# Kernel tuning notes

Measured on AMD Instinct MI355X. Metric: run time of the kernel, lower is better.

The kernel has to match this reference:

```python
import jax, jax.numpy as jnp
import numpy as np

B, N, C = 4, 4000, 91          # images, proposals/image, classes (incl. background)
H = W = 800                    # image shape
WX, WY, WW, WH = 10.0, 10.0, 5.0, 5.0   # bbox_reg_weights
BBOX_CLIP = float(np.log(1000.0 / 16.0))
SCORE_T = 0.05
NMS_T = 0.5
DETS = 100                     # detections_per_img
MIN_SIZE = 0.01
NEG = jnp.float32(-1e30)
M = N * (C - 1)                # candidates per image after dropping background


def setup_inputs() -> dict:
    key = jax.random.key(0)
    k1, k2, k3, k4 = jax.random.split(key, 4)
    class_logits = jax.random.normal(k1, (B * N, C), jnp.float32)
    box_regression = jax.random.normal(k2, (B * N, C * 4), jnp.float32)
    # valid proposals: x1<x2, y1<y2, inside the image
    ctr = jax.random.uniform(k3, (B, N, 2), jnp.float32, 0.0, 800.0)
    wh = jax.random.uniform(k4, (B, N, 2), jnp.float32, 16.0, 256.0)
    x1y1 = jnp.clip(ctr - 0.5 * wh, 0.0, 800.0)
    x2y2 = jnp.clip(ctr + 0.5 * wh, 0.0, 800.0)
    proposals = jnp.concatenate([x1y1, x2y2], axis=-1)
    return {"class_logits": class_logits, "box_regression": box_regression,
            "proposals": proposals}


def _decode(rel, props):
    # rel: [B,N,C,4] deltas, props: [B,N,4] -> per-class boxes [B,N,C,4]
    widths = props[..., 2] - props[..., 0]
    heights = props[..., 3] - props[..., 1]
    ctr_x = props[..., 0] + 0.5 * widths
    ctr_y = props[..., 1] + 0.5 * heights
    dx = rel[..., 0] / WX
    dy = rel[..., 1] / WY
    dw = jnp.minimum(rel[..., 2] / WW, BBOX_CLIP)
    dh = jnp.minimum(rel[..., 3] / WH, BBOX_CLIP)
    pcx = dx * widths[..., None] + ctr_x[..., None]
    pcy = dy * heights[..., None] + ctr_y[..., None]
    pw = jnp.exp(dw) * widths[..., None]
    ph = jnp.exp(dh) * heights[..., None]
    return jnp.stack([pcx - 0.5 * pw, pcy - 0.5 * ph,
                      pcx + 0.5 * pw, pcy + 0.5 * ph], axis=-1)


def _iou_one(box, boxes):
    # box [4] vs boxes [M,4]
    lt = jnp.maximum(box[:2], boxes[:, :2])
    rb = jnp.minimum(box[2:], boxes[:, 2:])
    wh = jnp.clip(rb - lt, 0.0)
    inter = wh[:, 0] * wh[:, 1]
    a1 = (box[2] - box[0]) * (box[3] - box[1])
    a2 = (boxes[:, 2] - boxes[:, 0]) * (boxes[:, 3] - boxes[:, 1])
    return inter / (a1 + a2 - inter)


def _nms_image(boxes_off, scores_m):
    # greedy NMS on class-offset boxes; returns DETS indices + validity flags
    idxs = jnp.arange(scores_m.shape[0])

    def step(scores_rem, _):
        best = jnp.argmax(scores_rem)
        bscore = scores_rem[best]
        iou = _iou_one(boxes_off[best], boxes_off)
        sup = (iou > NMS_T) | (idxs == best)
        return jnp.where(sup, NEG, scores_rem), (best, bscore > NEG * 0.5)

    _, (keep_idx, keep_ok) = jax.lax.scan(step, scores_m, None, length=DETS)
    return keep_idx, keep_ok


def reference(class_logits, box_regression, proposals):
    logits = class_logits.reshape(B, N, C)
    rel = box_regression.reshape(B, N, C, 4)
    boxes = _decode(rel, proposals)                       # [B,N,C,4]
    # clip_boxes_to_image
    boxes = jnp.stack([jnp.clip(boxes[..., 0], 0.0, W),
                       jnp.clip(boxes[..., 1], 0.0, H),
                       jnp.clip(boxes[..., 2], 0.0, W),
                       jnp.clip(boxes[..., 3], 0.0, H)], axis=-1)
    scores = jax.nn.softmax(logits, axis=-1)              # [B,N,C]
    # drop background class 0, flatten per-image candidates
    cand_boxes = boxes[:, :, 1:, :].reshape(B, M, 4)
    cand_scores = scores[:, :, 1:].reshape(B, M)
    labels = jnp.tile(jnp.arange(1, C, dtype=jnp.int32), N)   # [M]
    # score threshold + remove_small_boxes
    ws = cand_boxes[..., 2] - cand_boxes[..., 0]
    hs = cand_boxes[..., 3] - cand_boxes[..., 1]
    valid = (cand_scores > SCORE_T) & (ws >= MIN_SIZE) & (hs >= MIN_SIZE)
    scores_m = jnp.where(valid, cand_scores, NEG)
    # batched_nms: offset boxes per class so cross-class boxes never overlap
    offs = labels.astype(jnp.float32) * (W + 1.0)
    boxes_off = cand_boxes + offs[None, :, None]
    keep_idx, keep_ok = jax.vmap(_nms_image)(boxes_off, scores_m)  # [B,DETS]
    out_boxes = jnp.take_along_axis(cand_boxes, keep_idx[..., None], axis=1)
    out_scores = jnp.take_along_axis(cand_scores, keep_idx, axis=1)
    out_labels = labels[keep_idx]
    out_boxes = jnp.where(keep_ok[..., None], out_boxes, 0.0)
    out_scores = jnp.where(keep_ok, out_scores, 0.0)
    out_labels = jnp.where(keep_ok, out_labels, 0)
    return out_boxes, out_scores, out_labels, keep_ok
```

## Files before the change

kernel.cpp:

```cpp
#include <hip/hip_runtime.h>

#define Bc 4
#define Nc 4000
#define Cc 91
#define SEGW 20
#define BCAP 64
#define SELTGT 512
#define DETS 100
#define NBIN 4096
#define SELCAP 1024

typedef unsigned long long u64;

__device__ __forceinline__ float4 decode_box(const float4 r, float w, float h,
                                             float cx, float cy) {
    const float BBOX_CLIP = 4.135166556742356f;
    float dx = r.x / 10.f, dy = r.y / 10.f;
    float dw = fminf(r.z / 5.f, BBOX_CLIP);
    float dh = fminf(r.w / 5.f, BBOX_CLIP);
    float pcx = dx * w + cx, pcy = dy * h + cy;
    float pw = expf(dw) * w, ph = expf(dh) * h;
    float4 o;
    o.x = fminf(fmaxf(pcx - 0.5f * pw, 0.f), 800.f);
    o.y = fminf(fmaxf(pcy - 0.5f * ph, 0.f), 800.f);
    o.z = fminf(fmaxf(pcx + 0.5f * pw, 0.f), 800.f);
    o.w = fminf(fmaxf(pcy + 0.5f * ph, 0.f), 800.f);
    return o;
}

__global__ __launch_bounds__(256) void compact_k(
    const float* __restrict__ logits, const float* __restrict__ regs,
    const float* __restrict__ props, ulonglong2* __restrict__ pmask,
    unsigned* __restrict__ scoreseg, int* __restrict__ ghist) {
    if (blockIdx.x < 16) {
        int base = blockIdx.x * 1024;
#pragma unroll
        for (int j = 0; j < 4; ++j)
            ghist[base + j * 256 + threadIdx.x] = 0;
    }
    const int wv = threadIdx.x >> 6;
    const int ln = threadIdx.x & 63;
    const int pA = blockIdx.x * 8 + wv * 2;
    const int pB = pA + 1;

    const float* lA = logits + (size_t)pA * Cc;
    const float* lB = logits + (size_t)pB * Cc;
    float a0 = lA[ln];
    float b0 = lB[ln];
    float a1 = (ln < Cc - 64) ? lA[64 + ln] : -1e30f;
    float b1 = (ln < Cc - 64) ? lB[64 + ln] : -1e30f;
    const float4 prA = *reinterpret_cast<const float4*>(props + 4 * (size_t)pA);
    const float4 prB = *reinterpret_cast<const float4*>(props + 4 * (size_t)pB);

    float mA = fmaxf(a0, a1), mB = fmaxf(b0, b1);
#pragma unroll
    for (int off = 32; off; off >>= 1) {
        mA = fmaxf(mA, __shfl_xor(mA, off));
        mB = fmaxf(mB, __shfl_xor(mB, off));
    }
    float eA0 = expf(a0 - mA), eB0 = expf(b0 - mB);
    float eA1 = (ln < Cc - 64) ? expf(a1 - mA) : 0.f;
    float eB1 = (ln < Cc - 64) ? expf(b1 - mB) : 0.f;
    float sA = eA0 + eA1, sB = eB0 + eB1;
#pragma unroll
    for (int off = 32; off; off >>= 1) {
        sA += __shfl_xor(sA, off);
        sB += __shfl_xor(sB, off);
    }

    const float wA = prA.z - prA.x, hA = prA.w - prA.y;
    const float cxA = prA.x + 0.5f * wA, cyA = prA.y + 0.5f * hA;
    const float wB = prB.z - prB.x, hB = prB.w - prB.y;
    const float cxB = prB.x + 0.5f * wB, cyB = prB.y + 0.5f * hB;

    float vA0 = eA0 / sA, vB0 = eB0 / sB, vA1 = eA1 / sA, vB1 = eB1 / sB;
    bool fA0 = false, fA1 = false, fB0 = false, fB1 = false;
    if (ln >= 1 && vA0 > 0.05f) {
        float4 r = *reinterpret_cast<const float4*>(
            regs + ((size_t)pA * Cc + ln) * 4);
        float4 bx = decode_box(r, wA, hA, cxA, cyA);
        fA0 = (bx.z - bx.x >= 0.01f) && (bx.w - bx.y >= 0.01f);
    }
    if (ln >= 1 && vB0 > 0.05f) {
        float4 r = *reinterpret_cast<const float4*>(
            regs + ((size_t)pB * Cc + ln) * 4);
        float4 bx = decode_box(r, wB, hB, cxB, cyB);
        fB0 = (bx.z - bx.x >= 0.01f) && (bx.w - bx.y >= 0.01f);
    }
    if (ln < Cc - 64 && vA1 > 0.05f) {
        float4 r = *reinterpret_cast<const float4*>(
            regs + ((size_t)pA * Cc + 64 + ln) * 4);
        float4 bx = decode_box(r, wA, hA, cxA, cyA);
        fA1 = (bx.z - bx.x >= 0.01f) && (bx.w - bx.y >= 0.01f);
    }
    if (ln < Cc - 64 && vB1 > 0.05f) {
        float4 r = *reinterpret_cast<const float4*>(
            regs + ((size_t)pB * Cc + 64 + ln) * 4);
        float4 bx = decode_box(r, wB, hB, cxB, cyB);
        fB1 = (bx.z - bx.x >= 0.01f) && (bx.w - bx.y >= 0.01f);
    }

    const u64 below = (1ULL << ln) - 1ULL;
    u64 mA0 = __ballot(fA0), mA1 = __ballot(fA1);
    u64 mB0 = __ballot(fB0), mB1 = __ballot(fB1);
    int cA0 = __popcll(mA0), cB0 = __popcll(mB0);
    if (fA0) scoreseg[(size_t)pA * SEGW + __popcll(mA0 & below)] =
        __float_as_uint(vA0);
    if (fA1) scoreseg[(size_t)pA * SEGW + cA0 + __popcll(mA1 & below)] =
        __float_as_uint(vA1);
    if (fB0) scoreseg[(size_t)pB * SEGW + __popcll(mB0 & below)] =
        __float_as_uint(vB0);
    if (fB1) scoreseg[(size_t)pB * SEGW + cB0 + __popcll(mB1 & below)] =
        __float_as_uint(vB1);
    if (ln == 0) {
        pmask[pA] = make_ulonglong2(mA0, mA1);
        pmask[pB] = make_ulonglong2(mB0, mB1);
    }
}

__global__ __launch_bounds__(256) void hist_k(
    const ulonglong2* __restrict__ pmask, const unsigned* __restrict__ scoreseg,
    int* __restrict__ ghist) {
    __shared__ int hist[NBIN];
    const int b = blockIdx.x >> 4;
    const int sub = blockIdx.x & 15;
    const int t = threadIdx.x;
    for (int i = t; i < NBIN; i += 256) hist[i] = 0;
    __syncthreads();
    if (t < 250) {
        int p = b * Nc + sub * 250 + t;
        ulonglong2 pm = pmask[p];
        int nk = __popcll(pm.x) + __popcll(pm.y);
        for (int j = 0; j < nk; ++j)
            atomicAdd(&hist[scoreseg[(size_t)p * SEGW + j] >> 20], 1);
    }
    __syncthreads();
    for (int i = t; i < NBIN; i += 256) {
        int v = hist[i];
        if (v) atomicAdd(&ghist[b * NBIN + i], v);
    }
}

__global__ __launch_bounds__(256) void thresh_k(const int* __restrict__ ghist,
                                               int* __restrict__ thr,
                                               int* __restrict__ bcnt) {
    {
        const int t = threadIdx.x;
        if (t < Bc * Cc - 256) bcnt[256 + t] = 0;
        bcnt[t] = 0;
    }
    const int wv = threadIdx.x >> 6;
    const int ln = threadIdx.x & 63;
    const int* h = ghist + wv * NBIN;
    int loc[64];
    int tot = 0;
#pragma unroll
    for (int j = 0; j < 64; ++j) { loc[j] = h[ln * 64 + j]; tot += loc[j]; }
    int inc = tot;
#pragma unroll
    for (int off = 1; off < 64; off <<= 1) {
        int v = __shfl_down(inc, off);
        if (ln + off < 64) inc += v;
    }
    int cum = inc - tot;
    int myThr = -1;
#pragma unroll
    for (int j = 63; j >= 0; --j) {
        if (cum < SELTGT && cum + loc[j] >= SELTGT) myThr = ln * 64 + j;
        cum += loc[j];
    }
#pragma unroll
    for (int off = 32; off; off >>= 1)
        myThr = max(myThr, __shfl_xor(myThr, off));
    if (ln == 0) thr[wv] = (myThr < 0) ? 0 : myThr;
}

__global__ __launch_bounds__(256) void select_k(
    const ulonglong2* __restrict__ pmask, const unsigned* __restrict__ scoreseg,
    const int* __restrict__ thr, u64* __restrict__ bucket,
    int* __restrict__ bcnt) {
    const int p = blockIdx.x * 256 + threadIdx.x;
    if (p >= Bc * Nc) return;
    const ulonglong2 pm = pmask[p];
    if ((pm.x | pm.y) == 0ULL) return;
    const int b = p / Nc;
    const int n = p - b * Nc;
    const int th = thr[b];
    int idx = 0;
#pragma unroll
    for (int rnd = 0; rnd < 2; ++rnd) {
        u64 mm = rnd ? pm.y : pm.x;
        while (mm) {
            int j = __ffsll((long long)mm) - 1; mm &= mm - 1;
            int c = j + rnd * 64;
            unsigned sb = scoreseg[(size_t)p * SEGW + idx]; ++idx;
            if ((int)(sb >> 20) >= th) {
                unsigned m = (unsigned)(n * 90 + (c - 1));
                u64 key = ((u64)sb << 32) | ((u64)(1048575u - m) << 12) | (u64)c;
                int sl = atomicAdd(&bcnt[b * Cc + c], 1);
                if (sl < BCAP) bucket[(b * Cc + c) * BCAP + sl] = key;
            }
        }
    }
}

__global__ __launch_bounds__(64) void nmsc_k(
    u64* __restrict__ bucket, const int* __restrict__ bcnt,
    const float* __restrict__ regs, const float* __restrict__ props,
    int* __restrict__ kkc) {
    const int b = blockIdx.x / (Cc - 1);
    const int c = 1 + blockIdx.x % (Cc - 1);
    const int ln = threadIdx.x;
    const int nc = min(bcnt[b * Cc + c], BCAP);
    bool alive = ln < nc;
    u64 lk = alive ? bucket[(b * Cc + c) * BCAP + ln] : 0ULL;
    float4 bx = make_float4(0.f, 0.f, 0.f, 0.f);
    float area = 0.f;
    if (alive) {
        int m = 1048575 - (int)((lk >> 12) & 0xFFFFFULL);
        int n = m / (Cc - 1);
        int p = b * Nc + n;
        const float4 pr = *reinterpret_cast<const float4*>(props + 4 * (size_t)p);
        float w = pr.z - pr.x, h = pr.w - pr.y;
        float cx = pr.x + 0.5f * w, cy = pr.y + 0.5f * h;
        const float4 r = *reinterpret_cast<const float4*>(
            regs + ((size_t)p * Cc + c) * 4);
        bx = decode_box(r, w, h, cx, cy);
        float off_ = (float)c * 801.0f;
        bx.x += off_; bx.y += off_; bx.z += off_; bx.w += off_;
        area = (bx.z - bx.x) * (bx.w - bx.y);
    }

    int nk = 0;
    for (;;) {
        u64 m = alive ? lk : 0ULL;
#pragma unroll
        for (int off = 32; off; off >>= 1) {
            u64 o = __shfl_xor(m, off);
            m = (o > m) ? o : m;
        }
        if (m == 0ULL) break;
        u64 wmask = __ballot(alive && lk == m);
        int wl = __ffsll((long long)wmask) - 1;
        if (ln == wl) bucket[(b * Cc + c) * BCAP + nk] = m;
        ++nk;
        float wx1 = __shfl(bx.x, wl), wy1 = __shfl(bx.y, wl);
        float wx2 = __shfl(bx.z, wl), wy2 = __shfl(bx.w, wl);
        float wa = __shfl(area, wl);
        if (alive) {
            if (lk == m) {
                alive = false;
            } else {
                float iw = fmaxf(fminf(wx2, bx.z) - fmaxf(wx1, bx.x), 0.f);
                float ih = fmaxf(fminf(wy2, bx.w) - fmaxf(wy1, bx.y), 0.f);
                float inter = iw * ih;
                float iou = inter / (wa + area - inter);
                if (iou > 0.5f) alive = false;
            }
        }
    }
    if (ln == 0) kkc[b * Cc + c] = nk;
}

__global__ __launch_bounds__(1024) void top100_k(
    const u64* __restrict__ bucket, const int* __restrict__ kkc,
    const float* __restrict__ regs, const float* __restrict__ props,
    float* __restrict__ out) {
    __shared__ u64 sKey[SELCAP];
    __shared__ u64 sTop[DETS];
    __shared__ int cnts[Cc], offs[Cc + 1];
    const int b = blockIdx.x, t = threadIdx.x;
    const int ln = t & 63, wv = t >> 6;

    if (t < Cc)
        cnts[t] = (t == 0) ? 0 : min(max(kkc[b * Cc + t], 0), BCAP);
    if (t < DETS) sTop[t] = 0ULL;
    __syncthreads();
    if (t == 0) {
        int acc = 0;
        for (int c = 0; c < Cc; ++c) { offs[c] = acc; acc += cnts[c]; }
        offs[Cc] = acc;
    }
    __syncthreads();
    const int total = min(offs[Cc], SELCAP);

    for (int c = wv; c < Cc; c += 16) {
        int k = cnts[c];
        if (ln < k) {
            int d = offs[c] + ln;
            if (d >= 0 && d < SELCAP)
                sKey[d] = bucket[(b * Cc + c) * BCAP + ln];
        }
    }
    __syncthreads();

    for (int i = t; i < total; i += 1024) {
        u64 k = sKey[i];
        int r = 0;
#pragma unroll 4
        for (int j = 0; j < total; ++j) r += (sKey[j] > k) ? 1 : 0;
        if (r < DETS) sTop[r] = k;
    }
    __syncthreads();

    if (t < DETS) {
        int o = b * DETS + t;
        u64 k = sTop[t];
        float* ob = out + (size_t)o * 4;
        if (k != 0ULL) {
            int lab = (int)(k & 0xFFFULL);
            int m = 1048575 - (int)((k >> 12) & 0xFFFFFULL);
            int n = m / (Cc - 1);
            int c = m - n * (Cc - 1) + 1;
            int p = b * Nc + n;
            const float4 pr =
                *reinterpret_cast<const float4*>(props + 4 * (size_t)p);
            const float w = pr.z - pr.x, h = pr.w - pr.y;
            const float cx = pr.x + 0.5f * w, cy = pr.y + 0.5f * h;
            const float4 r4 = *reinterpret_cast<const float4*>(
                regs + ((size_t)p * Cc + c) * 4);
            float4 bx = decode_box(r4, w, h, cx, cy);
            ob[0] = bx.x; ob[1] = bx.y; ob[2] = bx.z; ob[3] = bx.w;
            out[Bc * DETS * 4 + o] = __uint_as_float((unsigned)(k >> 32));
            out[Bc * DETS * 5 + o] = (float)lab;
            out[Bc * DETS * 6 + o] = 1.0f;
        } else {
            ob[0] = ob[1] = ob[2] = ob[3] = 0.f;
            out[Bc * DETS * 4 + o] = 0.f;
            out[Bc * DETS * 5 + o] = 0.f;
            out[Bc * DETS * 6 + o] = 0.f;
        }
    }
}

extern "C" void kernel_launch(void* const* d_in, const int* in_sizes, int n_in,
                              void* d_out, int out_size, void* d_ws, size_t ws_size,
                              hipStream_t stream) {
    const float* logits = (const float*)d_in[0];
    const float* regs   = (const float*)d_in[1];
    const float* props  = (const float*)d_in[2];
    float* out = (float*)d_out;

    char* ws = (char*)d_ws;
    size_t o = 0;
    ulonglong2* pmask = (ulonglong2*)(ws + o); o += (size_t)Bc * Nc * 16;
    unsigned* scoreseg = (unsigned*)(ws + o);  o += (size_t)Bc * Nc * SEGW * 4;
    u64* bucket  = (u64*)(ws + o);             o += (size_t)Bc * Cc * BCAP * 8;
    int* ghist   = (int*)(ws + o);             o += (size_t)Bc * NBIN * 4;
    int* bcnt    = (int*)(ws + o);             o += (size_t)Bc * Cc * 4;
    int* kkc     = (int*)(ws + o);             o += (size_t)Bc * Cc * 4;
    int* thr     = (int*)(ws + o);

    hipLaunchKernelGGL(compact_k, dim3(Bc * Nc / 8), dim3(256), 0, stream,
                       logits, regs, props, pmask, scoreseg, ghist);
    hipLaunchKernelGGL(hist_k, dim3(Bc * 16), dim3(256), 0, stream,
                       pmask, scoreseg, ghist);
    hipLaunchKernelGGL(thresh_k, dim3(1), dim3(256), 0, stream, ghist, thr, bcnt);
    hipLaunchKernelGGL(select_k, dim3((Bc * Nc + 255) / 256), dim3(256), 0,
                       stream, pmask, scoreseg, thr, bucket, bcnt);
    hipLaunchKernelGGL(nmsc_k, dim3(Bc * (Cc - 1)), dim3(64), 0, stream,
                       bucket, bcnt, regs, props, kkc);
    hipLaunchKernelGGL(top100_k, dim3(Bc), dim3(1024), 0, stream,
                       bucket, kkc, regs, props, out);
}
```

Baseline: 55.73 us.

## Fuse threshold into select and per-class NMS into top-100 kernel

Cuts the pipeline from six launches to four. Each select block now recomputes its image's histogram threshold itself, and the per-class NMS runs inside the per-image top-100 kernel, using shared-memory buckets loaded once. bcnt zeroing moves into compact_k. This removes launch and inter-kernel gaps, but NMS now runs on only 4 blocks of 16 waves, each wave looping over about 6 classes serially, instead of 360 parallel single-wave blocks. The per-block threshold scan is also repeated 16 times per image.

```diff
diff --git a/kernel.cpp b/kernel.cpp
--- a/kernel.cpp
+++ b/kernel.cpp
@@ -31,12 +31,17 @@
 __global__ __launch_bounds__(256) void compact_k(
     const float* __restrict__ logits, const float* __restrict__ regs,
     const float* __restrict__ props, ulonglong2* __restrict__ pmask,
-    unsigned* __restrict__ scoreseg, int* __restrict__ ghist) {
+    unsigned* __restrict__ scoreseg, int* __restrict__ ghist,
+    int* __restrict__ bcnt) {
     if (blockIdx.x < 16) {
         int base = blockIdx.x * 1024;
 #pragma unroll
         for (int j = 0; j < 4; ++j)
             ghist[base + j * 256 + threadIdx.x] = 0;
+    } else if (blockIdx.x == 16) {
+        int t = threadIdx.x;
+        bcnt[t] = 0;
+        if (t < Bc * Cc - 256) bcnt[256 + t] = 0;
     }
     const int wv = threadIdx.x >> 6;
     const int ln = threadIdx.x & 63;
@@ -141,155 +146,155 @@
     }
 }
 
-__global__ __launch_bounds__(256) void thresh_k(const int* __restrict__ ghist,
-                                               int* __restrict__ thr,
-                                               int* __restrict__ bcnt) {
-    {
-        const int t = threadIdx.x;
-        if (t < Bc * Cc - 256) bcnt[256 + t] = 0;
-        bcnt[t] = 0;
-    }
-    const int wv = threadIdx.x >> 6;
-    const int ln = threadIdx.x & 63;
-    const int* h = ghist + wv * NBIN;
-    int loc[64];
-    int tot = 0;
-#pragma unroll
-    for (int j = 0; j < 64; ++j) { loc[j] = h[ln * 64 + j]; tot += loc[j]; }
-    int inc = tot;
-#pragma unroll
-    for (int off = 1; off < 64; off <<= 1) {
-        int v = __shfl_down(inc, off);
-        if (ln + off < 64) inc += v;
-    }
-    int cum = inc - tot;
-    int myThr = -1;
-#pragma unroll
-    for (int j = 63; j >= 0; --j) {
-        if (cum < SELTGT && cum + loc[j] >= SELTGT) myThr = ln * 64 + j;
-        cum += loc[j];
-    }
-#pragma unroll
-    for (int off = 32; off; off >>= 1)
-        myThr = max(myThr, __shfl_xor(myThr, off));
-    if (ln == 0) thr[wv] = (myThr < 0) ? 0 : myThr;
-}
-
-__global__ __launch_bounds__(256) void select_k(
+__global__ __launch_bounds__(256) void selthr_k(
     const ulonglong2* __restrict__ pmask, const unsigned* __restrict__ scoreseg,
-    const int* __restrict__ thr, u64* __restrict__ bucket,
+    const int* __restrict__ ghist, u64* __restrict__ bucket,
     int* __restrict__ bcnt) {
-    const int p = blockIdx.x * 256 + threadIdx.x;
-    if (p >= Bc * Nc) return;
-    const ulonglong2 pm = pmask[p];
-    if ((pm.x | pm.y) == 0ULL) return;
-    const int b = p / Nc;
-    const int n = p - b * Nc;
-    const int th = thr[b];
-    int idx = 0;
-#pragma unroll
-    for (int rnd = 0; rnd < 2; ++rnd) {
-        u64 mm = rnd ? pm.y : pm.x;
-        while (mm) {
-            int j = __ffsll((long long)mm) - 1; mm &= mm - 1;
-            int c = j + rnd * 64;
-            unsigned sb = scoreseg[(size_t)p * SEGW + idx]; ++idx;
-            if ((int)(sb >> 20) >= th) {
-                unsigned m = (unsigned)(n * 90 + (c - 1));
-                u64 key = ((u64)sb << 32) | ((u64)(1048575u - m) << 12) | (u64)c;
-                int sl = atomicAdd(&bcnt[b * Cc + c], 1);
-                if (sl < BCAP) bucket[(b * Cc + c) * BCAP + sl] = key;
+    __shared__ int thrS;
+    const int b = blockIdx.x >> 4;
+    const int sub = blockIdx.x & 15;
+    const int t = threadIdx.x;
+
+    if (t < 64) {
+        const int ln = t;
+        const int* h = ghist + b * NBIN;
+        int loc[64];
+        int tot = 0;
+#pragma unroll
+        for (int j = 0; j < 64; ++j) { loc[j] = h[ln * 64 + j]; tot += loc[j]; }
+        int inc = tot;
+#pragma unroll
+        for (int off = 1; off < 64; off <<= 1) {
+            int v = __shfl_down(inc, off);
+            if (ln + off < 64) inc += v;
+        }
+        int cum = inc - tot;
+        int myThr = -1;
+#pragma unroll
+        for (int j = 63; j >= 0; --j) {
+            if (cum < SELTGT && cum + loc[j] >= SELTGT) myThr = ln * 64 + j;
+            cum += loc[j];
+        }
+#pragma unroll
+        for (int off = 32; off; off >>= 1)
+            myThr = max(myThr, __shfl_xor(myThr, off));
+        if (ln == 0) thrS = (myThr < 0) ? 0 : myThr;
+    }
+    __syncthreads();
+    const int th = thrS;
+
+    if (t < 250) {
+        int p = b * Nc + sub * 250 + t;
+        const ulonglong2 pm = pmask[p];
+        if (pm.x | pm.y) {
+            const int n = p - b * Nc;
+            int idx = 0;
+#pragma unroll
+            for (int rnd = 0; rnd < 2; ++rnd) {
+                u64 mm = rnd ? pm.y : pm.x;
+                while (mm) {
+                    int j = __ffsll((long long)mm) - 1; mm &= mm - 1;
+                    int c = j + rnd * 64;
+                    unsigned sb = scoreseg[(size_t)p * SEGW + idx]; ++idx;
+                    if ((int)(sb >> 20) >= th) {
+                        unsigned m = (unsigned)(n * 90 + (c - 1));
+                        u64 key = ((u64)sb << 32) |
+                                  ((u64)(1048575u - m) << 12) | (u64)c;
+                        int sl = atomicAdd(&bcnt[b * Cc + c], 1);
+                        if (sl < BCAP) bucket[(b * Cc + c) * BCAP + sl] = key;
+                    }
+                }
             }
         }
     }
 }
 
-__global__ __launch_bounds__(64) void nmsc_k(
-    u64* __restrict__ bucket, const int* __restrict__ bcnt,
-    const float* __restrict__ regs, const float* __restrict__ props,
-    int* __restrict__ kkc) {
-    const int b = blockIdx.x / (Cc - 1);
-    const int c = 1 + blockIdx.x % (Cc - 1);
-    const int ln = threadIdx.x;
-    const int nc = min(bcnt[b * Cc + c], BCAP);
-    bool alive = ln < nc;
-    u64 lk = alive ? bucket[(b * Cc + c) * BCAP + ln] : 0ULL;
-    float4 bx = make_float4(0.f, 0.f, 0.f, 0.f);
-    float area = 0.f;
-    if (alive) {
-        int m = 1048575 - (int)((lk >> 12) & 0xFFFFFULL);
-        int n = m / (Cc - 1);
-        int p = b * Nc + n;
-        const float4 pr = *reinterpret_cast<const float4*>(props + 4 * (size_t)p);
-        float w = pr.z - pr.x, h = pr.w - pr.y;
-        float cx = pr.x + 0.5f * w, cy = pr.y + 0.5f * h;
-        const float4 r = *reinterpret_cast<const float4*>(
-            regs + ((size_t)p * Cc + c) * 4);
-        bx = decode_box(r, w, h, cx, cy);
-        float off_ = (float)c * 801.0f;
-        bx.x += off_; bx.y += off_; bx.z += off_; bx.w += off_;
-        area = (bx.z - bx.x) * (bx.w - bx.y);
-    }
-
-    int nk = 0;
-    for (;;) {
-        u64 m = alive ? lk : 0ULL;
-#pragma unroll
-        for (int off = 32; off; off >>= 1) {
-            u64 o = __shfl_xor(m, off);
-            m = (o > m) ? o : m;
-        }
-        if (m == 0ULL) break;
-        u64 wmask = __ballot(alive && lk == m);
-        int wl = __ffsll((long long)wmask) - 1;
-        if (ln == wl) bucket[(b * Cc + c) * BCAP + nk] = m;
-        ++nk;
-        float wx1 = __shfl(bx.x, wl), wy1 = __shfl(bx.y, wl);
-        float wx2 = __shfl(bx.z, wl), wy2 = __shfl(bx.w, wl);
-        float wa = __shfl(area, wl);
-        if (alive) {
-            if (lk == m) {
-                alive = false;
-            } else {
-                float iw = fmaxf(fminf(wx2, bx.z) - fmaxf(wx1, bx.x), 0.f);
-                float ih = fmaxf(fminf(wy2, bx.w) - fmaxf(wy1, bx.y), 0.f);
-                float inter = iw * ih;
-                float iou = inter / (wa + area - inter);
-                if (iou > 0.5f) alive = false;
-            }
-        }
-    }
-    if (ln == 0) kkc[b * Cc + c] = nk;
-}
-
-__global__ __launch_bounds__(1024) void top100_k(
-    const u64* __restrict__ bucket, const int* __restrict__ kkc,
+__global__ __launch_bounds__(1024) void nmstop_k(
+    const u64* __restrict__ bucket, const int* __restrict__ bcnt,
     const float* __restrict__ regs, const float* __restrict__ props,
     float* __restrict__ out) {
+    __shared__ u64 sBkt[Cc][BCAP];
     __shared__ u64 sKey[SELCAP];
     __shared__ u64 sTop[DETS];
-    __shared__ int cnts[Cc], offs[Cc + 1];
+    __shared__ int cnts[Cc], kk[Cc], offs[Cc + 1];
     const int b = blockIdx.x, t = threadIdx.x;
     const int ln = t & 63, wv = t >> 6;
 
-    if (t < Cc)
-        cnts[t] = (t == 0) ? 0 : min(max(kkc[b * Cc + t], 0), BCAP);
+    if (t < Cc) cnts[t] = min(max(bcnt[b * Cc + t], 0), BCAP);
     if (t < DETS) sTop[t] = 0ULL;
-    __syncthreads();
+    for (int i = t; i < Cc * BCAP; i += 1024)
+        sBkt[0][i] = bucket[(size_t)b * Cc * BCAP + i];
+    __syncthreads();
+
+    for (int cm1 = wv; cm1 < Cc - 1; cm1 += 16) {
+        const int c = cm1 + 1;
+        const int nc = cnts[c];
+        bool alive = ln < nc;
+        u64 lk = alive ? sBkt[c][ln] : 0ULL;
+        float4 bx = make_float4(0.f, 0.f, 0.f, 0.f);
+        float area = 0.f;
+        if (alive) {
+            int m = 1048575 - (int)((lk >> 12) & 0xFFFFFULL);
+            int n = m / (Cc - 1);
+            int p = b * Nc + n;
+            const float4 pr =
+                *reinterpret_cast<const float4*>(props + 4 * (size_t)p);
+            float w = pr.z - pr.x, h = pr.w - pr.y;
+            float cx = pr.x + 0.5f * w, cy = pr.y + 0.5f * h;
+            const float4 r = *reinterpret_cast<const float4*>(
+                regs + ((size_t)p * Cc + c) * 4);
+            bx = decode_box(r, w, h, cx, cy);
+            float off_ = (float)c * 801.0f;
+            bx.x += off_; bx.y += off_; bx.z += off_; bx.w += off_;
+            area = (bx.z - bx.x) * (bx.w - bx.y);
+        }
+        int nk = 0;
+        for (;;) {
+            u64 m = alive ? lk : 0ULL;
+#pragma unroll
+            for (int off = 32; off; off >>= 1) {
+                u64 o = __shfl_xor(m, off);
+                m = (o > m) ? o : m;
+            }
+            if (m == 0ULL) break;
+            u64 wmask = __ballot(alive && lk == m);
+            int wl = __ffsll((long long)wmask) - 1;
+            if (ln == wl) sBkt[c][nk] = m;
+            ++nk;
+            float wx1 = __shfl(bx.x, wl), wy1 = __shfl(bx.y, wl);
+            float wx2 = __shfl(bx.z, wl), wy2 = __shfl(bx.w, wl);
+            float wa = __shfl(area, wl);
+            if (alive) {
+                if (lk == m) {
+                    alive = false;
+                } else {
+                    float iw = fmaxf(fminf(wx2, bx.z) - fmaxf(wx1, bx.x), 0.f);
+                    float ih = fmaxf(fminf(wy2, bx.w) - fmaxf(wy1, bx.y), 0.f);
+                    float inter = iw * ih;
+                    float iou = inter / (wa + area - inter);
+                    if (iou > 0.5f) alive = false;
+                }
+            }
+        }
+        if (ln == 0) kk[c] = nk;
+    }
+    __syncthreads();
+
     if (t == 0) {
         int acc = 0;
-        for (int c = 0; c < Cc; ++c) { offs[c] = acc; acc += cnts[c]; }
+        offs[0] = 0;
+        for (int c = 1; c < Cc; ++c) { offs[c] = acc; acc += kk[c]; }
         offs[Cc] = acc;
     }
     __syncthreads();
     const int total = min(offs[Cc], SELCAP);
 
-    for (int c = wv; c < Cc; c += 16) {
-        int k = cnts[c];
+    for (int cm1 = wv; cm1 < Cc - 1; cm1 += 16) {
+        const int c = cm1 + 1;
+        int k = kk[c];
         if (ln < k) {
             int d = offs[c] + ln;
-            if (d >= 0 && d < SELCAP)
-                sKey[d] = bucket[(b * Cc + c) * BCAP + ln];
+            if (d >= 0 && d < SELCAP) sKey[d] = sBkt[c][ln];
         }
     }
     __syncthreads();
@@ -348,18 +353,13 @@
     u64* bucket  = (u64*)(ws + o);             o += (size_t)Bc * Cc * BCAP * 8;
     int* ghist   = (int*)(ws + o);             o += (size_t)Bc * NBIN * 4;
     int* bcnt    = (int*)(ws + o);             o += (size_t)Bc * Cc * 4;
-    int* kkc     = (int*)(ws + o);             o += (size_t)Bc * Cc * 4;
-    int* thr     = (int*)(ws + o);
 
     hipLaunchKernelGGL(compact_k, dim3(Bc * Nc / 8), dim3(256), 0, stream,
-                       logits, regs, props, pmask, scoreseg, ghist);
+                       logits, regs, props, pmask, scoreseg, ghist, bcnt);
     hipLaunchKernelGGL(hist_k, dim3(Bc * 16), dim3(256), 0, stream,
                        pmask, scoreseg, ghist);
-    hipLaunchKernelGGL(thresh_k, dim3(1), dim3(256), 0, stream, ghist, thr, bcnt);
-    hipLaunchKernelGGL(select_k, dim3((Bc * Nc + 255) / 256), dim3(256), 0,
-                       stream, pmask, scoreseg, thr, bucket, bcnt);
-    hipLaunchKernelGGL(nmsc_k, dim3(Bc * (Cc - 1)), dim3(64), 0, stream,
-                       bucket, bcnt, regs, props, kkc);
-    hipLaunchKernelGGL(top100_k, dim3(Bc), dim3(1024), 0, stream,
-                       bucket, kkc, regs, props, out);
-}
+    hipLaunchKernelGGL(selthr_k, dim3(Bc * 16), dim3(256), 0, stream,
+                       pmask, scoreseg, ghist, bucket, bcnt);
+    hipLaunchKernelGGL(nmstop_k, dim3(Bc), dim3(1024), 0, stream,
+                       bucket, bcnt, regs, props, out);
+}
```

Measured after the change: 81.26 us. 1.46x slower.

## Fuse histogram, threshold and select kernels using a grid-wide atomic barrier

Applied to the files above, without the earlier changes.

Merges hist_k, thresh_k and select_k into one kernel of 64 blocks. The blocks synchronise through a global done counter with a spin-wait, then each block computes its image's threshold locally and selects candidates from its own proposal slice. Zeroing of bcnt and the done counter moves into compact_k. This removes two kernel launches and their gaps, but relies on all 64 blocks being co-resident and adds spin-wait and redundant threshold work in each block.

```diff
diff --git a/kernel.cpp b/kernel.cpp
--- a/kernel.cpp
+++ b/kernel.cpp
@@ -31,12 +31,18 @@
 __global__ __launch_bounds__(256) void compact_k(
     const float* __restrict__ logits, const float* __restrict__ regs,
     const float* __restrict__ props, ulonglong2* __restrict__ pmask,
-    unsigned* __restrict__ scoreseg, int* __restrict__ ghist) {
+    unsigned* __restrict__ scoreseg, int* __restrict__ ghist,
+    int* __restrict__ bcnt, int* __restrict__ done) {
     if (blockIdx.x < 16) {
         int base = blockIdx.x * 1024;
 #pragma unroll
         for (int j = 0; j < 4; ++j)
             ghist[base + j * 256 + threadIdx.x] = 0;
+    } else if (blockIdx.x == 16) {
+        int t = threadIdx.x;
+        bcnt[t] = 0;
+        if (t < Bc * Cc - 256) bcnt[256 + t] = 0;
+        if (t == 0) *done = 0;
     }
     const int wv = threadIdx.x >> 6;
     const int ln = threadIdx.x & 63;
@@ -118,13 +124,16 @@
     }
 }
 
-__global__ __launch_bounds__(256) void hist_k(
+__global__ __launch_bounds__(256) void histsel_k(
     const ulonglong2* __restrict__ pmask, const unsigned* __restrict__ scoreseg,
-    int* __restrict__ ghist) {
+    int* __restrict__ ghist, int* __restrict__ done,
+    u64* __restrict__ bucket, int* __restrict__ bcnt) {
     __shared__ int hist[NBIN];
+    __shared__ int thrS;
     const int b = blockIdx.x >> 4;
     const int sub = blockIdx.x & 15;
     const int t = threadIdx.x;
+
     for (int i = t; i < NBIN; i += 256) hist[i] = 0;
     __syncthreads();
     if (t < 250) {
@@ -139,66 +148,65 @@
         int v = hist[i];
         if (v) atomicAdd(&ghist[b * NBIN + i], v);
     }
-}
-
-__global__ __launch_bounds__(256) void thresh_k(const int* __restrict__ ghist,
-                                               int* __restrict__ thr,
-                                               int* __restrict__ bcnt) {
-    {
-        const int t = threadIdx.x;
-        if (t < Bc * Cc - 256) bcnt[256 + t] = 0;
-        bcnt[t] = 0;
-    }
-    const int wv = threadIdx.x >> 6;
-    const int ln = threadIdx.x & 63;
-    const int* h = ghist + wv * NBIN;
-    int loc[64];
-    int tot = 0;
-#pragma unroll
-    for (int j = 0; j < 64; ++j) { loc[j] = h[ln * 64 + j]; tot += loc[j]; }
-    int inc = tot;
-#pragma unroll
-    for (int off = 1; off < 64; off <<= 1) {
-        int v = __shfl_down(inc, off);
-        if (ln + off < 64) inc += v;
-    }
-    int cum = inc - tot;
-    int myThr = -1;
-#pragma unroll
-    for (int j = 63; j >= 0; --j) {
-        if (cum < SELTGT && cum + loc[j] >= SELTGT) myThr = ln * 64 + j;
-        cum += loc[j];
-    }
-#pragma unroll
-    for (int off = 32; off; off >>= 1)
-        myThr = max(myThr, __shfl_xor(myThr, off));
-    if (ln == 0) thr[wv] = (myThr < 0) ? 0 : myThr;
-}
-
-__global__ __launch_bounds__(256) void select_k(
-    const ulonglong2* __restrict__ pmask, const unsigned* __restrict__ scoreseg,
-    const int* __restrict__ thr, u64* __restrict__ bucket,
-    int* __restrict__ bcnt) {
-    const int p = blockIdx.x * 256 + threadIdx.x;
-    if (p >= Bc * Nc) return;
-    const ulonglong2 pm = pmask[p];
-    if ((pm.x | pm.y) == 0ULL) return;
-    const int b = p / Nc;
-    const int n = p - b * Nc;
-    const int th = thr[b];
-    int idx = 0;
-#pragma unroll
-    for (int rnd = 0; rnd < 2; ++rnd) {
-        u64 mm = rnd ? pm.y : pm.x;
-        while (mm) {
-            int j = __ffsll((long long)mm) - 1; mm &= mm - 1;
-            int c = j + rnd * 64;
-            unsigned sb = scoreseg[(size_t)p * SEGW + idx]; ++idx;
-            if ((int)(sb >> 20) >= th) {
-                unsigned m = (unsigned)(n * 90 + (c - 1));
-                u64 key = ((u64)sb << 32) | ((u64)(1048575u - m) << 12) | (u64)c;
-                int sl = atomicAdd(&bcnt[b * Cc + c], 1);
-                if (sl < BCAP) bucket[(b * Cc + c) * BCAP + sl] = key;
+    __syncthreads();
+
+    if (t == 0) {
+        __threadfence();
+        atomicAdd(done, 1);
+        while (atomicAdd(done, 0) < 64) __builtin_amdgcn_s_sleep(8);
+        __threadfence();
+    }
+    __syncthreads();
+
+    if (t < 64) {
+        const int ln = t;
+        const int* h = ghist + b * NBIN;
+        int loc[64];
+        int tot = 0;
+#pragma unroll
+        for (int j = 0; j < 64; ++j) { loc[j] = h[ln * 64 + j]; tot += loc[j]; }
+        int inc = tot;
+#pragma unroll
+        for (int off = 1; off < 64; off <<= 1) {
+            int v = __shfl_down(inc, off);
+            if (ln + off < 64) inc += v;
+        }
+        int cum = inc - tot;
+        int myThr = -1;
+#pragma unroll
+        for (int j = 63; j >= 0; --j) {
+            if (cum < SELTGT && cum + loc[j] >= SELTGT) myThr = ln * 64 + j;
+            cum += loc[j];
+        }
+#pragma unroll
+        for (int off = 32; off; off >>= 1)
+            myThr = max(myThr, __shfl_xor(myThr, off));
+        if (ln == 0) thrS = (myThr < 0) ? 0 : myThr;
+    }
+    __syncthreads();
+    const int th = thrS;
+
+    if (t < 250) {
+        int p = b * Nc + sub * 250 + t;
+        const ulonglong2 pm = pmask[p];
+        if (pm.x | pm.y) {
+            const int n = p - b * Nc;
+            int idx = 0;
+#pragma unroll
+            for (int rnd = 0; rnd < 2; ++rnd) {
+                u64 mm = rnd ? pm.y : pm.x;
+                while (mm) {
+                    int j = __ffsll((long long)mm) - 1; mm &= mm - 1;
+                    int c = j + rnd * 64;
+                    unsigned sb = scoreseg[(size_t)p * SEGW + idx]; ++idx;
+                    if ((int)(sb >> 20) >= th) {
+                        unsigned m = (unsigned)(n * 90 + (c - 1));
+                        u64 key = ((u64)sb << 32) |
+                                  ((u64)(1048575u - m) << 12) | (u64)c;
+                        int sl = atomicAdd(&bcnt[b * Cc + c], 1);
+                        if (sl < BCAP) bucket[(b * Cc + c) * BCAP + sl] = key;
+                    }
+                }
             }
         }
     }
@@ -349,15 +357,12 @@
     int* ghist   = (int*)(ws + o);             o += (size_t)Bc * NBIN * 4;
     int* bcnt    = (int*)(ws + o);             o += (size_t)Bc * Cc * 4;
     int* kkc     = (int*)(ws + o);             o += (size_t)Bc * Cc * 4;
-    int* thr     = (int*)(ws + o);
+    int* done    = (int*)(ws + o);
 
     hipLaunchKernelGGL(compact_k, dim3(Bc * Nc / 8), dim3(256), 0, stream,
-                       logits, regs, props, pmask, scoreseg, ghist);
-    hipLaunchKernelGGL(hist_k, dim3(Bc * 16), dim3(256), 0, stream,
-                       pmask, scoreseg, ghist);
-    hipLaunchKernelGGL(thresh_k, dim3(1), dim3(256), 0, stream, ghist, thr, bcnt);
-    hipLaunchKernelGGL(select_k, dim3((Bc * Nc + 255) / 256), dim3(256), 0,
-                       stream, pmask, scoreseg, thr, bucket, bcnt);
+                       logits, regs, props, pmask, scoreseg, ghist, bcnt, done);
+    hipLaunchKernelGGL(histsel_k, dim3(Bc * 16), dim3(256), 0, stream,
+                       pmask, scoreseg, ghist, done, bucket, bcnt);
     hipLaunchKernelGGL(nmsc_k, dim3(Bc * (Cc - 1)), dim3(64), 0, stream,
                        bucket, bcnt, regs, props, kkc);
     hipLaunchKernelGGL(top100_k, dim3(Bc), dim3(1024), 0, stream,
```

New measurement: 55.26 us. No clear change (-0.8%).
